# Optimization experiments

Measured on AMD Instinct MI355X. Metric: run time of the kernel, lower is better.

The kernel has to match this reference:

```python
import jax, jax.numpy as jnp
import numpy as np

B, C, H, W = 8, 512, 96, 96

def setup_inputs() -> dict:
    key = jax.random.key(0)
    k1, k2, k3, k4, k5 = jax.random.split(key, 5)
    s = 0.02
    return {
        "x": jax.random.normal(k1, (B, C, H, W), dtype=jnp.float32),
        "w_qkv": jax.random.normal(k2, (3 * C, C), dtype=jnp.float32) * s,
        "b_qkv": jax.random.normal(k3, (3 * C,), dtype=jnp.float32) * s,
        "w_proj": jax.random.normal(k4, (C, C), dtype=jnp.float32) * s,
        "b_proj": jax.random.normal(k5, (C,), dtype=jnp.float32) * s,
    }

def reference(x, w_qkv, b_qkv, w_proj, b_proj):
    b, c, h, w = x.shape
    n = h * w
    # 1x1 conv == pointwise linear over channels
    qkv = jnp.einsum('bchw,oc->bohw', x, w_qkv) + b_qkv[None, :, None, None]
    qkv = qkv.reshape(b, 3, c, n)
    q, k, v = qkv[:, 0], qkv[:, 1], qkv[:, 2]  # each [B, C, N]
    # channel attention: scores are [B, C, C]
    scale = 1.0 / (c ** 0.5)
    attn = jax.nn.softmax(jnp.einsum('bcn,bdn->bcd', q, k) * scale, axis=-1)
    out = jnp.einsum('bcd,bdn->bcn', attn, v).reshape(b, c, h, w)
    out = jnp.einsum('bchw,oc->bohw', out, w_proj) + b_proj[None, :, None, None]
    return out
```

## Files before the change

### kernel.cpp

```cpp
#include <hip/hip_runtime.h>

typedef unsigned short u16;
typedef unsigned long long u64;
typedef __bf16 bf16x8 __attribute__((ext_vector_type(8)));
typedef u16 us8 __attribute__((ext_vector_type(8)));
typedef u16 us4 __attribute__((ext_vector_type(4)));
typedef float floatx4 __attribute__((ext_vector_type(4)));
typedef float f32x4 __attribute__((ext_vector_type(4)));

__device__ inline float b2f(u16 u) {
  union { unsigned u; float f; } x; x.u = ((unsigned)u) << 16; return x.f;
}
__device__ inline u16 f2b(float f) {
  union { float f; unsigned u; } x; x.f = f;
  unsigned r = x.u + 0x7fffu + ((x.u >> 16) & 1u);
  return (u16)(r >> 16);
}

__device__ __forceinline__ void gl_lds16(const u16* g, void* l) {
  __builtin_amdgcn_global_load_lds(
      (const __attribute__((address_space(1))) void*)g,
      (__attribute__((address_space(3))) void*)l, 16, 0, 0);
}

__global__ __launch_bounds__(256)
void detect_dtype(const u16* __restrict__ x, int* __restrict__ flag, int force) {
  __shared__ float sm[4];
  const int t = threadIdx.x;
  float m = 0.f;
  for (int i = t; i < 4096; i += 256) {
    float v = fabsf(b2f(x[i]));
    if (v > m) m = v;
  }
#pragma unroll
  for (int o = 32; o; o >>= 1) m = fmaxf(m, __shfl_xor(m, o, 64));
  if ((t & 63) == 0) sm[t >> 6] = m;
  __syncthreads();
  if (t == 0) {
    float mm = fmaxf(fmaxf(sm[0], sm[1]), fmaxf(sm[2], sm[3]));
    *flag = (force >= 0) ? force : (mm > 1000.0f ? 1 : 0);
  }
}

__global__ __launch_bounds__(256)
void convert_bf16(const void* __restrict__ in, u16* __restrict__ out, long n,
                  const int* __restrict__ flag) {
  const long i = (blockIdx.x * 256L + threadIdx.x) * 8;
  if (i >= n) return;
  if (*flag) {
    const float* p = (const float*)in + i;
    f32x4 a = ((const f32x4*)p)[0];
    f32x4 b = ((const f32x4*)p)[1];
    us8 o;
#pragma unroll
    for (int j = 0; j < 4; j++) { o[j] = f2b(a[j]); o[j + 4] = f2b(b[j]); }
    *(us8*)(out + i) = o;
  } else {
    *(us8*)(out + i) = *((const us8*)in + (i >> 3));
  }
}

template <typename OutT>
__global__ __launch_bounds__(256)
void gemm_nt(const u16* __restrict__ A, long sA, int lda,
             const u16* __restrict__ B, long sB, int ldb,
             OutT* __restrict__ D, long sD, int ldd, int K) {
  __shared__ __align__(16) u16 As[64 * 32];
  __shared__ __align__(16) u16 Bs[64 * 32];
  const int bz = blockIdx.z;
  const u16* Ab = A + (long)bz * sA;
  const u16* Bb = B + (long)bz * sB;
  OutT* Db = D + (long)bz * sD;
  const int tid  = threadIdx.x;
  const int lane = tid & 63;
  const int wave = tid >> 6;
  const int wm = (wave >> 1) * 32, wn = (wave & 1) * 32;
  const int m0 = blockIdx.y * 64, n0 = blockIdx.x * 64;
  const int srow = tid >> 2;
  const int ss   = tid & 3;
  const int sco  = (ss ^ ((srow >> 1) & 3)) * 8;
  const int lr = lane & 15;
  const int rsw = (((lane >> 4) ^ ((lr >> 1) & 3)) * 8);
  char* asb = (char*)As + wave * 1024;
  char* bsb = (char*)Bs + wave * 1024;

  floatx4 acc[2][2];
#pragma unroll
  for (int i = 0; i < 2; i++)
#pragma unroll
    for (int j = 0; j < 2; j++) acc[i][j] = (floatx4){0.f, 0.f, 0.f, 0.f};

  for (int k0 = 0; k0 < K; k0 += 32) {
    __syncthreads();
    gl_lds16(&Ab[(long)(m0 + srow) * lda + k0 + sco], asb);
    gl_lds16(&Bb[(long)(n0 + srow) * ldb + k0 + sco], bsb);
    __syncthreads();
    bf16x8 af[2], bfr[2];
#pragma unroll
    for (int i = 0; i < 2; i++)
      af[i] = *(bf16x8*)&As[(wm + i * 16 + lr) * 32 + rsw];
#pragma unroll
    for (int i = 0; i < 2; i++)
      bfr[i] = *(bf16x8*)&Bs[(wn + i * 16 + lr) * 32 + rsw];
#pragma unroll
    for (int mi = 0; mi < 2; mi++)
#pragma unroll
      for (int ni = 0; ni < 2; ni++)
        acc[mi][ni] = __builtin_amdgcn_mfma_f32_16x16x32_bf16(
            af[mi], bfr[ni], acc[mi][ni], 0, 0, 0);
  }

  const int lc  = lane & 15;
  const int lr4 = (lane >> 4) * 4;
#pragma unroll
  for (int mi = 0; mi < 2; mi++) {
#pragma unroll
    for (int r = 0; r < 4; r++) {
      int gm = m0 + wm + mi * 16 + lr4 + r;
#pragma unroll
      for (int ni = 0; ni < 2; ni++) {
        int gn = n0 + wn + ni * 16 + lc;
        float v = acc[mi][ni][r];
        if constexpr (sizeof(OutT) == 4) Db[(long)gm * ldd + gn] = v;
        else                             Db[(long)gm * ldd + gn] = f2b(v);
      }
    }
  }
}

__device__ inline void tile_decode(int t, int& by, int& bx) {
  by = (int)((sqrtf((float)(8 * t + 1)) - 1.0f) * 0.5f);
  bx = t - (by * (by + 1)) / 2;
}

__global__ __launch_bounds__(256)
void gemm_xxt_splitk(const u16* __restrict__ X, float* __restrict__ P) {
  __shared__ __align__(16) u16 As[128 * 32];
  __shared__ __align__(16) u16 Bs[128 * 32];
  const int t  = blockIdx.x;
  const int bz = blockIdx.z >> 3;
  const int sp = blockIdx.z & 7;
  int by, bx;
  tile_decode(t, by, bx);
  const int m0 = by * 128, n0 = bx * 128;
  const u16* Xb = X + (long)bz * 512 * 9216;
  const int tid  = threadIdx.x;
  const int lane = tid & 63;
  const int wave = tid >> 6;
  const int wm = (wave >> 1) * 64, wn = (wave & 1) * 64;
  const int srow = tid >> 2;
  const int ss   = tid & 3;
  const int sco  = (ss ^ ((srow >> 1) & 3)) * 8;
  const int lr = lane & 15;
  const int rsw = (((lane >> 4) ^ ((lr >> 1) & 3)) * 8);
  char* asb = (char*)As + wave * 1024;
  char* bsb = (char*)Bs + wave * 1024;

  floatx4 acc[4][4];
#pragma unroll
  for (int i = 0; i < 4; i++)
#pragma unroll
    for (int j = 0; j < 4; j++) acc[i][j] = (floatx4){0.f, 0.f, 0.f, 0.f};

  const int k0beg = sp * 1152;
  for (int k0 = k0beg; k0 < k0beg + 1152; k0 += 32) {
    __syncthreads();
    gl_lds16(&Xb[(long)(m0 + srow) * 9216 + k0 + sco], asb);
    gl_lds16(&Xb[(long)(m0 + 64 + srow) * 9216 + k0 + sco], asb + 4096);
    gl_lds16(&Xb[(long)(n0 + srow) * 9216 + k0 + sco], bsb);
    gl_lds16(&Xb[(long)(n0 + 64 + srow) * 9216 + k0 + sco], bsb + 4096);
    __syncthreads();
    bf16x8 af[4], bfr[4];
#pragma unroll
    for (int i = 0; i < 4; i++)
      af[i] = *(bf16x8*)&As[(wm + i * 16 + lr) * 32 + rsw];
#pragma unroll
    for (int i = 0; i < 4; i++)
      bfr[i] = *(bf16x8*)&Bs[(wn + i * 16 + lr) * 32 + rsw];
#pragma unroll
    for (int mi = 0; mi < 4; mi++)
#pragma unroll
      for (int ni = 0; ni < 4; ni++)
        acc[mi][ni] = __builtin_amdgcn_mfma_f32_16x16x32_bf16(
            af[mi], bfr[ni], acc[mi][ni], 0, 0, 0);
  }

  float* Pb = P + ((long)(sp * 8 + bz) * 10 + t) * 16384;
  const int lc  = lane & 15;
  const int lr4 = (lane >> 4) * 4;
#pragma unroll
  for (int mi = 0; mi < 4; mi++)
#pragma unroll
    for (int r = 0; r < 4; r++) {
      int gm = wm + mi * 16 + lr4 + r;
#pragma unroll
      for (int ni = 0; ni < 4; ni++)
        Pb[gm * 128 + wn + ni * 16 + lc] = acc[mi][ni][r];
    }
}

__global__ __launch_bounds__(256)
void reduce_xxt(const float* __restrict__ P, u16* __restrict__ G) {
  __shared__ u16 tl[128][130];
  const int t = blockIdx.x, bz = blockIdx.y;
  int by, bx;
  tile_decode(t, by, bx);
  const int m0 = by * 128, n0 = bx * 128;
  u16* Gb = G + (long)bz * 512 * 512;
  for (int e = threadIdx.x; e < 4096; e += 256) {
    const int idx = e * 4;
    const int m = idx >> 7, n = idx & 127;
    f32x4 s = {0.f, 0.f, 0.f, 0.f};
#pragma unroll
    for (int sp = 0; sp < 8; sp++) {
      f32x4 v = *(const f32x4*)&P[(((long)sp * 8 + bz) * 10 + t) * 16384 + idx];
      s.x += v.x; s.y += v.y; s.z += v.z; s.w += v.w;
    }
    us4 o = {f2b(s.x), f2b(s.y), f2b(s.z), f2b(s.w)};
    *(us4*)&Gb[(long)(m0 + m) * 512 + n0 + n] = o;
    tl[m][n] = o[0]; tl[m][n + 1] = o[1]; tl[m][n + 2] = o[2]; tl[m][n + 3] = o[3];
  }
  if (m0 == n0) return;
  __syncthreads();
  for (int e = threadIdx.x; e < 4096; e += 256) {
    const int idx = e * 4;
    const int nr = idx >> 7, mc = idx & 127;
    us4 o = {tl[mc][nr], tl[mc + 1][nr], tl[mc + 2][nr], tl[mc + 3][nr]};
    *(us4*)&Gb[(long)(n0 + nr) * 512 + m0 + mc] = o;
  }
}

__global__ __launch_bounds__(256)
void gemm_nn_out(const u16* __restrict__ A, const u16* __restrict__ B,
                 const float* __restrict__ bias, void* __restrict__ Dout,
                 const int* __restrict__ flag) {
  __shared__ __align__(16)  u16 As[128 * 32];
  __shared__ __align__(128) u16 Bs[32 * 128];
  const int f = *flag;
  const int bz = blockIdx.z;
  const u16* Ab = A + (long)bz * 512 * 512;
  const u16* Bb = B + (long)bz * 512 * 9216;
  const float* cb = bias + bz * 512;
  const int tid  = threadIdx.x;
  const int lane = tid & 63;
  const int wave = tid >> 6;
  const int wm = (wave >> 1) * 64, wn = (wave & 1) * 64;
  const int m0 = blockIdx.y * 128, n0 = blockIdx.x * 128;
  const int srow = tid >> 2;
  const int ss   = tid & 3;
  const int sco  = (ss ^ ((srow >> 1) & 3)) * 8;
  const int lr = lane & 15;
  const int rsw = (((lane >> 4) ^ ((lr >> 1) & 3)) * 8);
  char* asb = (char*)As + wave * 1024;
  char* bsb = (char*)Bs + wave * 1024;
  const int bs_k = ((tid >> 3) & 7) * 4 + ((tid >> 1) & 3);
  const int bs_n = (tid >> 6) * 16 + (tid & 1) * 8;
  const unsigned bsBase = (unsigned)(size_t)(&Bs[0]);
  const unsigned trA = bsBase + (unsigned)((wn >> 4) * 1024 +
                       (lane >> 4) * 256 + (lane & 15) * 8);

  floatx4 acc[4][4];
#pragma unroll
  for (int i = 0; i < 4; i++)
#pragma unroll
    for (int j = 0; j < 4; j++) acc[i][j] = (floatx4){0.f, 0.f, 0.f, 0.f};

  for (int k0 = 0; k0 < 512; k0 += 32) {
    __syncthreads();
    gl_lds16(&Ab[(long)(m0 + srow) * 512 + k0 + sco], asb);
    gl_lds16(&Ab[(long)(m0 + 64 + srow) * 512 + k0 + sco], asb + 4096);
    const u16* bp = &Bb[(long)(k0 + bs_k) * 9216 + n0 + bs_n];
    gl_lds16(bp, bsb);
    gl_lds16(bp + 64, bsb + 4096);
    __syncthreads();
    bf16x8 af[4];
#pragma unroll
    for (int i = 0; i < 4; i++)
      af[i] = *(bf16x8*)&As[(wm + i * 16 + lr) * 32 + rsw];
    u64 blo[4], bhi[4];
#pragma unroll
    for (int ni = 0; ni < 4; ni++) {
      unsigned a = trA + ni * 1024;
      asm volatile("ds_read_b64_tr_b16 %0, %1" : "=v"(blo[ni]) : "v"(a));
      asm volatile("ds_read_b64_tr_b16 %0, %1 offset:128" : "=v"(bhi[ni]) : "v"(a));
    }
    asm volatile("s_waitcnt lgkmcnt(0)" ::: "memory");
    __builtin_amdgcn_sched_barrier(0);
    bf16x8 bfr[4];
#pragma unroll
    for (int ni = 0; ni < 4; ni++) {
      union { u64 q[2]; bf16x8 v; } u;
      u.q[0] = blo[ni]; u.q[1] = bhi[ni];
      bfr[ni] = u.v;
    }
#pragma unroll
    for (int mi = 0; mi < 4; mi++)
#pragma unroll
      for (int ni = 0; ni < 4; ni++)
        acc[mi][ni] = __builtin_amdgcn_mfma_f32_16x16x32_bf16(
            af[mi], bfr[ni], acc[mi][ni], 0, 0, 0);
  }

  const int lc  = lane & 15;
  const int lr4 = (lane >> 4) * 4;
  if (f) {
    float* Db = (float*)Dout + (long)bz * 512 * 9216;
#pragma unroll
    for (int mi = 0; mi < 4; mi++)
#pragma unroll
      for (int r = 0; r < 4; r++) {
        int gm = m0 + wm + mi * 16 + lr4 + r;
        float bv = cb[gm];
#pragma unroll
        for (int ni = 0; ni < 4; ni++)
          Db[(long)gm * 9216 + n0 + wn + ni * 16 + lc] = acc[mi][ni][r] + bv;
      }
  } else {
    u16* Db = (u16*)Dout + (long)bz * 512 * 9216;
#pragma unroll
    for (int mi = 0; mi < 4; mi++)
#pragma unroll
      for (int r = 0; r < 4; r++) {
        int gm = m0 + wm + mi * 16 + lr4 + r;
        float bv = cb[gm];
#pragma unroll
        for (int ni = 0; ni < 4; ni++)
          Db[(long)gm * 9216 + n0 + wn + ni * 16 + lc] = f2b(acc[mi][ni][r] + bv);
      }
  }
}

__global__ __launch_bounds__(256)
void rowsum(const u16* __restrict__ x, float* __restrict__ r) {
  const int row  = blockIdx.x * 4 + (threadIdx.x >> 6);
  const int lane = threadIdx.x & 63;
  const u16* p = x + (long)row * 9216;
  float s = 0.f;
#pragma unroll
  for (int t = 0; t < 18; t++) {
    us8 v = *(const us8*)&p[t * 512 + lane * 8];
#pragma unroll
    for (int e = 0; e < 8; e++) s += b2f(v[e]);
  }
#pragma unroll
  for (int o = 32; o; o >>= 1) s += __shfl_xor(s, o, 64);
  if (lane == 0) r[row] = s;
}

__global__ __launch_bounds__(256)
void matvec_uw(const u16* __restrict__ w_qkv, const float* __restrict__ r,
               float* __restrict__ u, float* __restrict__ w) {
  const int g = blockIdx.x * 256 + threadIdx.x;
  const int b = g >> 10;
  const int s = (g >> 9) & 1;
  const int i = g & 511;
  const u16* Wrow = w_qkv + (long)(s * 512 + i) * 512;
  const float* rb = r + b * 512;
  float acc = 0.f;
  for (int c = 0; c < 512; c++) acc += b2f(Wrow[c]) * rb[c];
  (s ? w : u)[b * 512 + i] = acc;
}

__global__ __launch_bounds__(256)
void cvec(const u16* __restrict__ w_proj, const float* __restrict__ y,
          const u16* __restrict__ b_proj, float* __restrict__ cv) {
  const int g = blockIdx.x * 256 + threadIdx.x;
  const int b = g >> 9;
  const int o = g & 511;
  const u16* Wrow = w_proj + (long)o * 512;
  const float* yb = y + b * 512;
  float acc = 0.f;
  for (int i = 0; i < 512; i++) acc += b2f(Wrow[i]) * yb[i];
  cv[b * 512 + o] = acc + b2f(b_proj[o]);
}

__global__ __launch_bounds__(256)
void softmax_rank1(const float* __restrict__ Score, const float* __restrict__ u,
                   const float* __restrict__ w, const u16* __restrict__ b_qkv,
                   u16* __restrict__ PT, float* __restrict__ y) {
  const int row  = blockIdx.x * 4 + (threadIdx.x >> 6);
  const int lane = threadIdx.x & 63;
  const int b = row >> 9, i = row & 511;
  const float scale = 0.04419417382415922f;
  const float* srow = Score + (long)row * 512;
  const float* wb = w + b * 512;
  const float bq_i = b2f(b_qkv[i]);
  const float uu = u[row] + 9216.0f * bq_i;
  float vals[8];
  float mx = -1e30f;
#pragma unroll
  for (int t = 0; t < 8; t++) {
    int j = lane + t * 64;
    float s = srow[j] + uu * b2f(b_qkv[512 + j]) + bq_i * wb[j];
    vals[t] = scale * s;
    mx = fmaxf(mx, vals[t]);
  }
#pragma unroll
  for (int o = 32; o; o >>= 1) mx = fmaxf(mx, __shfl_xor(mx, o, 64));
  float sum = 0.f, ys = 0.f;
#pragma unroll
  for (int t = 0; t < 8; t++) {
    int j = lane + t * 64;
    vals[t] = __expf(vals[t] - mx);
    sum += vals[t];
    ys += vals[t] * b2f(b_qkv[1024 + j]);
  }
#pragma unroll
  for (int o = 32; o; o >>= 1) sum += __shfl_xor(sum, o, 64);
#pragma unroll
  for (int o = 32; o; o >>= 1) ys += __shfl_xor(ys, o, 64);
  const float inv = 1.0f / sum;
#pragma unroll
  for (int t = 0; t < 8; t++) {
    int j = lane + t * 64;
    PT[(long)b * 512 * 512 + (long)j * 512 + i] = f2b(vals[t] * inv);
  }
  if (lane == 0) y[row] = ys * inv;
}

__global__ __launch_bounds__(256)
void transpose512(const u16* __restrict__ in, u16* __restrict__ out) {
  __shared__ u16 tile[32][33];
  const int c0 = blockIdx.x * 32, r0 = blockIdx.y * 32;
  const int tx = threadIdx.x, ty = threadIdx.y;
#pragma unroll
  for (int i = 0; i < 32; i += 8)
    tile[ty + i][tx] = in[(long)(r0 + ty + i) * 512 + c0 + tx];
  __syncthreads();
#pragma unroll
  for (int i = 0; i < 32; i += 8)
    out[(long)(c0 + ty + i) * 512 + r0 + tx] = tile[tx][ty + i];
}

extern "C" void kernel_launch(void* const* d_in, const int* in_sizes, int n_in,
                              void* d_out, int out_size, void* d_ws, size_t ws_size,
                              hipStream_t stream) {
  const long CN = 512L * 9216;
  const long SQ = 512L * 512;

  char* ws = (char*)d_ws;
  int*   flag  = (int*)ws;                      ws += 16;
  u16*   Gb    = (u16*)ws;                      ws += 8 * SQ * 2;
  u16*   T1    = (u16*)ws;                      ws += 8 * SQ * 2;
  u16*   PT    = (u16*)ws;                      ws += 8 * SQ * 2;
  u16*   T3    = (u16*)ws;                      ws += 8 * SQ * 2;
  u16*   Mm    = (u16*)ws;                      ws += 8 * SQ * 2;
  float* Score = (float*)ws;                    ws += 8 * SQ * 4;
  u16*   WvT   = (u16*)ws;                      ws += SQ * 2;
  float* r     = (float*)ws;                    ws += 8 * 512 * 4;
  float* u     = (float*)ws;                    ws += 8 * 512 * 4;
  float* w     = (float*)ws;                    ws += 8 * 512 * 4;
  float* y     = (float*)ws;                    ws += 8 * 512 * 4;
  float* cv    = (float*)ws;                    ws += 8 * 512 * 4;
  u16* xc      = (u16*)ws;                      ws += 8 * CN * 2;
  u16* wqkv_c  = (u16*)ws;                      ws += 1536L * 512 * 2;
  u16* bqkv_c  = (u16*)ws;                      ws += 1536L * 2;
  u16* wproj_c = (u16*)ws;                      ws += 512L * 512 * 2;
  u16* bproj_c = (u16*)ws;                      ws += 512L * 2;

  char* mark1 = ws;
  float* Psk  = (float*)ws;                     ws += 8L * 8 * 10 * 16384 * 4;

  const bool full  = ((size_t)(mark1 - (char*)d_ws) <= ws_size);
  const bool full2 = ((size_t)(ws    - (char*)d_ws) <= ws_size);

  if (full) {
    detect_dtype<<<1, 256, 0, stream>>>((const u16*)d_in[0], flag, -1);
    convert_bf16<<<18432, 256, 0, stream>>>(d_in[0], xc,      8 * CN,      flag);
    convert_bf16<<<384,   256, 0, stream>>>(d_in[1], wqkv_c,  1536L * 512, flag);
    convert_bf16<<<1,     256, 0, stream>>>(d_in[2], bqkv_c,  1536,        flag);
    convert_bf16<<<128,   256, 0, stream>>>(d_in[3], wproj_c, 512L * 512,  flag);
    convert_bf16<<<1,     256, 0, stream>>>(d_in[4], bproj_c, 512,         flag);
  } else {
    detect_dtype<<<1, 256, 0, stream>>>((const u16*)d_in[0], flag, 0);
    xc      = (u16*)d_in[0];
    wqkv_c  = (u16*)d_in[1];
    bqkv_c  = (u16*)d_in[2];
    wproj_c = (u16*)d_in[3];
    bproj_c = (u16*)d_in[4];
  }

  const u16* Wq = wqkv_c;
  const u16* Wk = wqkv_c + 512 * 512;
  const u16* Wv = wqkv_c + 1024 * 512;

  if (full2) {
    gemm_xxt_splitk<<<dim3(10, 1, 64), 256, 0, stream>>>(xc, Psk);
    reduce_xxt<<<dim3(10, 8), 256, 0, stream>>>(Psk, Gb);
  } else {
    gemm_nt<u16><<<dim3(8, 8, 8), 256, 0, stream>>>(
        xc, CN, 9216, xc, CN, 9216, Gb, SQ, 512, 9216);
  }
  rowsum<<<1024, 256, 0, stream>>>(xc, r);
  matvec_uw<<<32, 256, 0, stream>>>(wqkv_c, r, u, w);
  gemm_nt<u16><<<dim3(8, 8, 8), 256, 0, stream>>>(
      Wq, 0, 512, Gb, SQ, 512, T1, SQ, 512, 512);
  gemm_nt<float><<<dim3(8, 8, 8), 256, 0, stream>>>(
      T1, SQ, 512, Wk, 0, 512, Score, SQ, 512, 512);
  softmax_rank1<<<1024, 256, 0, stream>>>(Score, u, w, bqkv_c, PT, y);
  transpose512<<<dim3(16, 16), dim3(32, 8), 0, stream>>>(Wv, WvT);
  gemm_nt<u16><<<dim3(8, 8, 8), 256, 0, stream>>>(
      wproj_c, 0, 512, PT, SQ, 512, T3, SQ, 512, 512);
  gemm_nt<u16><<<dim3(8, 8, 8), 256, 0, stream>>>(
      T3, SQ, 512, WvT, 0, 512, Mm, SQ, 512, 512);
  cvec<<<16, 256, 0, stream>>>(wproj_c, y, bproj_c, cv);
  gemm_nn_out<<<dim3(72, 4, 8), 256, 0, stream>>>(Mm, xc, cv, d_out, flag);
}
```

Measured before the change: 550.4 us.

## Double-buffer GEMM LDS tiles, fuse rowsum into convert, wave-parallel matvecs

Adds two-stage LDS double buffering to gemm_nt, the split-K X·Xᵀ GEMM and the output GEMM, so the global-to-LDS load for the next K tile is issued while MFMAs run on the current tile. It also fuses the row sum of x into the bf16 conversion pass using wave reductions and atomics, which removes a separate full read of x. The two small matvec kernels are rewritten to use one wave per output row with a shuffle reduction, replacing one thread per output that looped over 512 elements. Doubling LDS per block may lower occupancy, and the atomic row sums make the summation order nondeterministic.

```diff
diff --git a/kernel.cpp b/kernel.cpp
--- a/kernel.cpp
+++ b/kernel.cpp
@@ -40,6 +40,12 @@
     float mm = fmaxf(fmaxf(sm[0], sm[1]), fmaxf(sm[2], sm[3]));
     *flag = (force >= 0) ? force : (mm > 1000.0f ? 1 : 0);
   }
+}
+
+__global__ __launch_bounds__(256)
+void zerof(float* __restrict__ p, int n) {
+  int i = blockIdx.x * 256 + threadIdx.x;
+  if (i < n) p[i] = 0.f;
 }
 
 __global__ __launch_bounds__(256)
@@ -60,13 +66,39 @@
   }
 }
 
+__global__ __launch_bounds__(256)
+void convert_x_rowsum(const void* __restrict__ in, u16* __restrict__ out,
+                      const int* __restrict__ flag, float* __restrict__ r) {
+  const long i = (blockIdx.x * 256L + threadIdx.x) * 8;
+  us8 o;
+  if (*flag) {
+    const float* p = (const float*)in + i;
+    f32x4 a = ((const f32x4*)p)[0];
+    f32x4 b = ((const f32x4*)p)[1];
+#pragma unroll
+    for (int j = 0; j < 4; j++) { o[j] = f2b(a[j]); o[j + 4] = f2b(b[j]); }
+  } else {
+    o = *((const us8*)in + (i >> 3));
+  }
+  *(us8*)(out + i) = o;
+  float s = 0.f;
+#pragma unroll
+  for (int j = 0; j < 8; j++) s += b2f(o[j]);
+#pragma unroll
+  for (int off = 32; off; off >>= 1) s += __shfl_xor(s, off, 64);
+  if ((threadIdx.x & 63) == 0) {
+    int row = (int)(i / 9216);
+    atomicAdd(&r[row], s);
+  }
+}
+
 template <typename OutT>
 __global__ __launch_bounds__(256)
 void gemm_nt(const u16* __restrict__ A, long sA, int lda,
              const u16* __restrict__ B, long sB, int ldb,
              OutT* __restrict__ D, long sD, int ldd, int K) {
-  __shared__ __align__(16) u16 As[64 * 32];
-  __shared__ __align__(16) u16 Bs[64 * 32];
+  __shared__ __align__(16) u16 As[2][64 * 32];
+  __shared__ __align__(16) u16 Bs[2][64 * 32];
   const int bz = blockIdx.z;
   const u16* Ab = A + (long)bz * sA;
   const u16* Bb = B + (long)bz * sB;
@@ -81,8 +113,6 @@
   const int sco  = (ss ^ ((srow >> 1) & 3)) * 8;
   const int lr = lane & 15;
   const int rsw = (((lane >> 4) ^ ((lr >> 1) & 3)) * 8);
-  char* asb = (char*)As + wave * 1024;
-  char* bsb = (char*)Bs + wave * 1024;
 
   floatx4 acc[2][2];
 #pragma unroll
@@ -90,24 +120,30 @@
 #pragma unroll
     for (int j = 0; j < 2; j++) acc[i][j] = (floatx4){0.f, 0.f, 0.f, 0.f};
 
-  for (int k0 = 0; k0 < K; k0 += 32) {
-    __syncthreads();
-    gl_lds16(&Ab[(long)(m0 + srow) * lda + k0 + sco], asb);
-    gl_lds16(&Bb[(long)(n0 + srow) * ldb + k0 + sco], bsb);
-    __syncthreads();
+  const int nt = K >> 5;
+  auto stage = [&](int buf, int k0) {
+    gl_lds16(&Ab[(long)(m0 + srow) * lda + k0 + sco], (char*)As[buf] + wave * 1024);
+    gl_lds16(&Bb[(long)(n0 + srow) * ldb + k0 + sco], (char*)Bs[buf] + wave * 1024);
+  };
+  stage(0, 0);
+  __syncthreads();
+  for (int t = 0; t < nt; t++) {
+    const int cur = t & 1;
+    if (t + 1 < nt) stage(cur ^ 1, (t + 1) << 5);
     bf16x8 af[2], bfr[2];
 #pragma unroll
     for (int i = 0; i < 2; i++)
-      af[i] = *(bf16x8*)&As[(wm + i * 16 + lr) * 32 + rsw];
+      af[i] = *(bf16x8*)&As[cur][(wm + i * 16 + lr) * 32 + rsw];
 #pragma unroll
     for (int i = 0; i < 2; i++)
-      bfr[i] = *(bf16x8*)&Bs[(wn + i * 16 + lr) * 32 + rsw];
+      bfr[i] = *(bf16x8*)&Bs[cur][(wn + i * 16 + lr) * 32 + rsw];
 #pragma unroll
     for (int mi = 0; mi < 2; mi++)
 #pragma unroll
       for (int ni = 0; ni < 2; ni++)
         acc[mi][ni] = __builtin_amdgcn_mfma_f32_16x16x32_bf16(
             af[mi], bfr[ni], acc[mi][ni], 0, 0, 0);
+    __syncthreads();
   }
 
   const int lc  = lane & 15;
@@ -135,8 +171,8 @@
 
 __global__ __launch_bounds__(256)
 void gemm_xxt_splitk(const u16* __restrict__ X, float* __restrict__ P) {
-  __shared__ __align__(16) u16 As[128 * 32];
-  __shared__ __align__(16) u16 Bs[128 * 32];
+  __shared__ __align__(16) u16 As[2][128 * 32];
+  __shared__ __align__(16) u16 Bs[2][128 * 32];
   const int t  = blockIdx.x;
   const int bz = blockIdx.z >> 3;
   const int sp = blockIdx.z & 7;
@@ -153,8 +189,6 @@
   const int sco  = (ss ^ ((srow >> 1) & 3)) * 8;
   const int lr = lane & 15;
   const int rsw = (((lane >> 4) ^ ((lr >> 1) & 3)) * 8);
-  char* asb = (char*)As + wave * 1024;
-  char* bsb = (char*)Bs + wave * 1024;
 
   floatx4 acc[4][4];
 #pragma unroll
@@ -163,26 +197,31 @@
     for (int j = 0; j < 4; j++) acc[i][j] = (floatx4){0.f, 0.f, 0.f, 0.f};
 
   const int k0beg = sp * 1152;
-  for (int k0 = k0beg; k0 < k0beg + 1152; k0 += 32) {
-    __syncthreads();
-    gl_lds16(&Xb[(long)(m0 + srow) * 9216 + k0 + sco], asb);
-    gl_lds16(&Xb[(long)(m0 + 64 + srow) * 9216 + k0 + sco], asb + 4096);
-    gl_lds16(&Xb[(long)(n0 + srow) * 9216 + k0 + sco], bsb);
-    gl_lds16(&Xb[(long)(n0 + 64 + srow) * 9216 + k0 + sco], bsb + 4096);
-    __syncthreads();
+  auto stage = [&](int buf, int k0) {
+    gl_lds16(&Xb[(long)(m0 + srow) * 9216 + k0 + sco], (char*)As[buf] + wave * 1024);
+    gl_lds16(&Xb[(long)(m0 + 64 + srow) * 9216 + k0 + sco], (char*)As[buf] + 4096 + wave * 1024);
+    gl_lds16(&Xb[(long)(n0 + srow) * 9216 + k0 + sco], (char*)Bs[buf] + wave * 1024);
+    gl_lds16(&Xb[(long)(n0 + 64 + srow) * 9216 + k0 + sco], (char*)Bs[buf] + 4096 + wave * 1024);
+  };
+  stage(0, k0beg);
+  __syncthreads();
+  for (int tt = 0; tt < 36; tt++) {
+    const int cur = tt & 1;
+    if (tt + 1 < 36) stage(cur ^ 1, k0beg + ((tt + 1) << 5));
     bf16x8 af[4], bfr[4];
 #pragma unroll
     for (int i = 0; i < 4; i++)
-      af[i] = *(bf16x8*)&As[(wm + i * 16 + lr) * 32 + rsw];
+      af[i] = *(bf16x8*)&As[cur][(wm + i * 16 + lr) * 32 + rsw];
 #pragma unroll
     for (int i = 0; i < 4; i++)
-      bfr[i] = *(bf16x8*)&Bs[(wn + i * 16 + lr) * 32 + rsw];
+      bfr[i] = *(bf16x8*)&Bs[cur][(wn + i * 16 + lr) * 32 + rsw];
 #pragma unroll
     for (int mi = 0; mi < 4; mi++)
 #pragma unroll
       for (int ni = 0; ni < 4; ni++)
         acc[mi][ni] = __builtin_amdgcn_mfma_f32_16x16x32_bf16(
             af[mi], bfr[ni], acc[mi][ni], 0, 0, 0);
+    __syncthreads();
   }
 
   float* Pb = P + ((long)(sp * 8 + bz) * 10 + t) * 16384;
@@ -234,8 +273,8 @@
 void gemm_nn_out(const u16* __restrict__ A, const u16* __restrict__ B,
                  const float* __restrict__ bias, void* __restrict__ Dout,
                  const int* __restrict__ flag) {
-  __shared__ __align__(16)  u16 As[128 * 32];
-  __shared__ __align__(128) u16 Bs[32 * 128];
+  __shared__ __align__(16)  u16 As[2][128 * 32];
+  __shared__ __align__(128) u16 Bs[2][32 * 128];
   const int f = *flag;
   const int bz = blockIdx.z;
   const u16* Ab = A + (long)bz * 512 * 512;
@@ -251,11 +290,9 @@
   const int sco  = (ss ^ ((srow >> 1) & 3)) * 8;
   const int lr = lane & 15;
   const int rsw = (((lane >> 4) ^ ((lr >> 1) & 3)) * 8);
-  char* asb = (char*)As + wave * 1024;
-  char* bsb = (char*)Bs + wave * 1024;
   const int bs_k = ((tid >> 3) & 7) * 4 + ((tid >> 1) & 3);
   const int bs_n = (tid >> 6) * 16 + (tid & 1) * 8;
-  const unsigned bsBase = (unsigned)(size_t)(&Bs[0]);
+  const unsigned bsBase = (unsigned)(size_t)(&Bs[0][0]);
   const unsigned trA = bsBase + (unsigned)((wn >> 4) * 1024 +
                        (lane >> 4) * 256 + (lane & 15) * 8);
 
@@ -265,22 +302,26 @@
 #pragma unroll
     for (int j = 0; j < 4; j++) acc[i][j] = (floatx4){0.f, 0.f, 0.f, 0.f};
 
-  for (int k0 = 0; k0 < 512; k0 += 32) {
-    __syncthreads();
-    gl_lds16(&Ab[(long)(m0 + srow) * 512 + k0 + sco], asb);
-    gl_lds16(&Ab[(long)(m0 + 64 + srow) * 512 + k0 + sco], asb + 4096);
+  auto stage = [&](int buf, int k0) {
+    gl_lds16(&Ab[(long)(m0 + srow) * 512 + k0 + sco], (char*)As[buf] + wave * 1024);
+    gl_lds16(&Ab[(long)(m0 + 64 + srow) * 512 + k0 + sco], (char*)As[buf] + 4096 + wave * 1024);
     const u16* bp = &Bb[(long)(k0 + bs_k) * 9216 + n0 + bs_n];
-    gl_lds16(bp, bsb);
-    gl_lds16(bp + 64, bsb + 4096);
-    __syncthreads();
+    gl_lds16(bp, (char*)Bs[buf] + wave * 1024);
+    gl_lds16(bp + 64, (char*)Bs[buf] + 4096 + wave * 1024);
+  };
+  stage(0, 0);
+  __syncthreads();
+  for (int t = 0; t < 16; t++) {
+    const int cur = t & 1;
+    if (t + 1 < 16) stage(cur ^ 1, (t + 1) << 5);
     bf16x8 af[4];
 #pragma unroll
     for (int i = 0; i < 4; i++)
-      af[i] = *(bf16x8*)&As[(wm + i * 16 + lr) * 32 + rsw];
+      af[i] = *(bf16x8*)&As[cur][(wm + i * 16 + lr) * 32 + rsw];
     u64 blo[4], bhi[4];
 #pragma unroll
     for (int ni = 0; ni < 4; ni++) {
-      unsigned a = trA + ni * 1024;
+      unsigned a = trA + cur * 8192 + ni * 1024;
       asm volatile("ds_read_b64_tr_b16 %0, %1" : "=v"(blo[ni]) : "v"(a));
       asm volatile("ds_read_b64_tr_b16 %0, %1 offset:128" : "=v"(bhi[ni]) : "v"(a));
     }
@@ -299,6 +340,7 @@
       for (int ni = 0; ni < 4; ni++)
         acc[mi][ni] = __builtin_amdgcn_mfma_f32_16x16x32_bf16(
             af[mi], bfr[ni], acc[mi][ni], 0, 0, 0);
+    __syncthreads();
   }
 
   const int lc  = lane & 15;
@@ -350,28 +392,42 @@
 __global__ __launch_bounds__(256)
 void matvec_uw(const u16* __restrict__ w_qkv, const float* __restrict__ r,
                float* __restrict__ u, float* __restrict__ w) {
-  const int g = blockIdx.x * 256 + threadIdx.x;
+  const int g = blockIdx.x * 4 + (threadIdx.x >> 6);
+  const int lane = threadIdx.x & 63;
   const int b = g >> 10;
   const int s = (g >> 9) & 1;
   const int i = g & 511;
   const u16* Wrow = w_qkv + (long)(s * 512 + i) * 512;
   const float* rb = r + b * 512;
-  float acc = 0.f;
-  for (int c = 0; c < 512; c++) acc += b2f(Wrow[c]) * rb[c];
-  (s ? w : u)[b * 512 + i] = acc;
+  us8 wv = *(const us8*)&Wrow[lane * 8];
+  f32x4 r0 = *(const f32x4*)&rb[lane * 8];
+  f32x4 r1 = *(const f32x4*)&rb[lane * 8 + 4];
+  float acc = b2f(wv[0]) * r0.x + b2f(wv[1]) * r0.y + b2f(wv[2]) * r0.z +
+              b2f(wv[3]) * r0.w + b2f(wv[4]) * r1.x + b2f(wv[5]) * r1.y +
+              b2f(wv[6]) * r1.z + b2f(wv[7]) * r1.w;
+#pragma unroll
+  for (int o = 32; o; o >>= 1) acc += __shfl_xor(acc, o, 64);
+  if (lane == 0) (s ? w : u)[b * 512 + i] = acc;
 }
 
 __global__ __launch_bounds__(256)
 void cvec(const u16* __restrict__ w_proj, const float* __restrict__ y,
           const u16* __restrict__ b_proj, float* __restrict__ cv) {
-  const int g = blockIdx.x * 256 + threadIdx.x;
+  const int g = blockIdx.x * 4 + (threadIdx.x >> 6);
+  const int lane = threadIdx.x & 63;
   const int b = g >> 9;
   const int o = g & 511;
   const u16* Wrow = w_proj + (long)o * 512;
   const float* yb = y + b * 512;
-  float acc = 0.f;
-  for (int i = 0; i < 512; i++) acc += b2f(Wrow[i]) * yb[i];
-  cv[b * 512 + o] = acc + b2f(b_proj[o]);
+  us8 wv = *(const us8*)&Wrow[lane * 8];
+  f32x4 y0 = *(const f32x4*)&yb[lane * 8];
+  f32x4 y1 = *(const f32x4*)&yb[lane * 8 + 4];
+  float acc = b2f(wv[0]) * y0.x + b2f(wv[1]) * y0.y + b2f(wv[2]) * y0.z +
+              b2f(wv[3]) * y0.w + b2f(wv[4]) * y1.x + b2f(wv[5]) * y1.y +
+              b2f(wv[6]) * y1.z + b2f(wv[7]) * y1.w;
+#pragma unroll
+  for (int off = 32; off; off >>= 1) acc += __shfl_xor(acc, off, 64);
+  if (lane == 0) cv[b * 512 + o] = acc + b2f(b_proj[o]);
 }
 
 __global__ __launch_bounds__(256)
@@ -466,7 +522,8 @@
 
   if (full) {
     detect_dtype<<<1, 256, 0, stream>>>((const u16*)d_in[0], flag, -1);
-    convert_bf16<<<18432, 256, 0, stream>>>(d_in[0], xc,      8 * CN,      flag);
+    zerof<<<16, 256, 0, stream>>>(r, 4096);
+    convert_x_rowsum<<<18432, 256, 0, stream>>>(d_in[0], xc, flag, r);
     convert_bf16<<<384,   256, 0, stream>>>(d_in[1], wqkv_c,  1536L * 512, flag);
     convert_bf16<<<1,     256, 0, stream>>>(d_in[2], bqkv_c,  1536,        flag);
     convert_bf16<<<128,   256, 0, stream>>>(d_in[3], wproj_c, 512L * 512,  flag);
@@ -478,6 +535,7 @@
     bqkv_c  = (u16*)d_in[2];
     wproj_c = (u16*)d_in[3];
     bproj_c = (u16*)d_in[4];
+    rowsum<<<1024, 256, 0, stream>>>(xc, r);
   }
 
   const u16* Wq = wqkv_c;
@@ -491,8 +549,7 @@
     gemm_nt<u16><<<dim3(8, 8, 8), 256, 0, stream>>>(
         xc, CN, 9216, xc, CN, 9216, Gb, SQ, 512, 9216);
   }
-  rowsum<<<1024, 256, 0, stream>>>(xc, r);
-  matvec_uw<<<32, 256, 0, stream>>>(wqkv_c, r, u, w);
+  matvec_uw<<<2048, 256, 0, stream>>>(wqkv_c, r, u, w);
   gemm_nt<u16><<<dim3(8, 8, 8), 256, 0, stream>>>(
       Wq, 0, 512, Gb, SQ, 512, T1, SQ, 512, 512);
   gemm_nt<float><<<dim3(8, 8, 8), 256, 0, stream>>>(
@@ -503,6 +560,6 @@
       wproj_c, 0, 512, PT, SQ, 512, T3, SQ, 512, 512);
   gemm_nt<u16><<<dim3(8, 8, 8), 256, 0, stream>>>(
       T3, SQ, 512, WvT, 0, 512, Mm, SQ, 512, 512);
-  cvec<<<16, 256, 0, stream>>>(wproj_c, y, bproj_c, cv);
+  cvec<<<1024, 256, 0, stream>>>(wproj_c, y, bproj_c, cv);
   gemm_nn_out<<<dim3(72, 4, 8), 256, 0, stream>>>(Mm, xc, cv, d_out, flag);
 }
```

Measured after the change: 504.3 us. 1.09x faster.
